# Kernel tuning notes

Measured on AMD Instinct MI355X. Metric: run time of the kernel, lower is better.

## Reference

```python
import jax, jax.numpy as jnp
import numpy as np

B, L, H, C, K, S = 32, 512, 336, 321, 8, 8   # batch, seq_len, pred_len, channels, leaders, states
FREQ = H // 2 + 1                            # 169
G = 2 * K + 1                                # filter groups
TEMP = 1.0
EPS = 1e-5


def setup_inputs() -> dict:
    key = jax.random.key(0)
    ks = jax.random.split(key, 12)
    x = jax.random.normal(ks[0], (B, L, C), jnp.float32)
    leader_ids = jax.random.randint(ks[1], (B, C, K), 0, C)
    shift = jax.random.randint(ks[2], (B, C, K), 0, L)
    r = jax.random.normal(ks[3], (B, C, K), jnp.float32)
    # backbone linear: seq_len -> pred_len
    Wb = jax.random.normal(ks[4], (H, L), jnp.float32) * float(1.0 / np.sqrt(L))
    bb = jnp.zeros((H,), jnp.float32)
    # factory classifier: (L + K) features -> state_num logits
    Wc = jax.random.normal(ks[5], (S, L + K), jnp.float32) * float(1.0 / np.sqrt(L + K))
    bc = jnp.zeros((S,), jnp.float32)
    # state prototype filters (complex, stored as re/im): [S, 2K+1, FREQ]
    states_re = jax.random.normal(ks[6], (S, G, FREQ), jnp.float32) * float(1.0 / np.sqrt(S))
    states_im = jax.random.normal(ks[7], (S, G, FREQ), jnp.float32) * float(1.0 / np.sqrt(S))
    # complex mix layer: 3*FREQ -> FREQ
    Wm_re = jax.random.normal(ks[8], (FREQ, 3 * FREQ), jnp.float32) * float(1.0 / np.sqrt(3 * FREQ))
    Wm_im = jax.random.normal(ks[9], (FREQ, 3 * FREQ), jnp.float32) * float(1.0 / np.sqrt(3 * FREQ))
    bm_re = jnp.zeros((FREQ,), jnp.float32)
    bm_im = jnp.zeros((FREQ,), jnp.float32)
    return dict(x=x, r=r, Wb=Wb, bb=bb, Wc=Wc, bc=bc,
                states_re=states_re, states_im=states_im,
                Wm_re=Wm_re, Wm_im=Wm_im, bm_re=bm_re, bm_im=bm_im,
                leader_ids=leader_ids, shift=shift)


def reference(x, r, Wb, bb, Wc, bc, states_re, states_im, Wm_re, Wm_im, bm_re, bm_im, leader_ids, shift):
    xc = jnp.transpose(x, (0, 2, 1))                      # [B,C,L]
    mu = xc.mean(-1, keepdims=True)
    norm = jnp.sqrt(xc.var(-1, keepdims=True) + EPS)
    xn = (xc - mu) / norm                                 # instance_norm
    y_hat = jnp.einsum('bcl,hl->bch', xn, Wb) + bb        # backbone [B,C,H]

    # --- shifted_leader_seq (torch.no_grad) ---
    full = jax.lax.stop_gradient(jnp.concatenate([xn, y_hat], -1))      # [B,C,L+H]
    lead_full = full[jnp.arange(B)[:, None, None], leader_ids]          # [B,C,K,L+H]
    t_idx = (L - shift)[..., None] + jnp.arange(H)                      # [B,C,K,H]
    seq_shifted = jnp.take_along_axis(lead_full, t_idx, axis=-1)        # [B,C,K,H]
    r = jax.lax.stop_gradient(r)

    # softmax leader weights with leading constant-one slot
    ones = jnp.ones((B, C, 1), xn.dtype)
    r_soft = jax.nn.softmax(jnp.concatenate([ones, jnp.abs(r)], -1) / TEMP, axis=-1)  # [B,C,K+1]

    # --- factory: state-mixed complex filters ---
    feat = jnp.concatenate([xn, r_soft[..., 1:]], -1)                   # [B,C,L+K]
    p = jax.nn.softmax(jnp.einsum('bcf,sf->bcs', feat, Wc) + bc, axis=-1)
    states = states_re + 1j * states_im                                 # [S,G,FREQ]
    filters = jnp.einsum('bcs,sgf->bcgf', p, states)                    # [B,C,2K+1,FREQ]

    # --- FFT filter multiply-sum + inverse FFT mix ---
    y_hat_f = jnp.fft.rfft(y_hat)                                       # [B,C,FREQ]
    seq_shifted_f = jnp.fft.rfft(seq_shifted) * filters[:, :, :K]       # [B,C,K,FREQ]
    seq_diff_f = (seq_shifted_f - y_hat_f[:, :, None]) * filters[:, :, K:-1]
    yh_f = y_hat_f * filters[:, :, -1]
    z = jnp.concatenate([seq_shifted_f.sum(2), seq_diff_f.sum(2), yh_f], -1)  # [B,C,3*FREQ]
    Wm = Wm_re + 1j * Wm_im
    mixed = jnp.einsum('bcf,gf->bcg', z, Wm) + (bm_re + 1j * bm_im)     # [B,C,FREQ]
    y_hat = y_hat + jnp.fft.irfft(mixed, n=H)

    y = y_hat * norm + mu
    return jnp.transpose(y, (0, 2, 1))                                  # [B,H,C]
```

## Files before the change

kernel.cpp:

```cpp
#include <hip/hip_runtime.h>
#include <math.h>

#define B_ 32
#define L_ 512
#define H_ 336
#define C_ 321
#define K_ 8
#define S_ 8
#define FREQ_ 169
#define G_ 17
#define LHB_ 848
#define F_FEAT 520
#define EPS_ 1e-5f
#define BCN_ (B_ * C_)
#define DZB_ 7

#ifndef M_PIf
#define M_PIf 3.14159265358979323846f
#endif

typedef __attribute__((ext_vector_type(8))) short short8v;
typedef __attribute__((ext_vector_type(4))) float f32x4;

__device__ __forceinline__ unsigned short f2bf(float x) {
    unsigned u = __builtin_bit_cast(unsigned, x);
    u += 0x7FFFu + ((u >> 16) & 1u);
    return (unsigned short)(u >> 16);
}
__device__ __forceinline__ float bf2f(unsigned short h) {
    return __builtin_bit_cast(float, (unsigned)h << 16);
}


__global__ void k_prep_dft(unsigned short* __restrict__ T) {
    int blk = blockIdx.x, kc = blk / 22, nt = blk % 22, lane = threadIdx.x;
    int n = nt * 16 + (lane & 15);
    int kb = kc * 32 + (lane >> 4) * 8;
    int f = n >> 1;
    unsigned short* dst = T + (size_t)blk * 512 + lane * 8;
    for (int i = 0; i < 8; ++i) {
        int k = kb + i;
        float val = 0.f;
        if (k < H_ && n < 2 * FREQ_) {
            int m = (k * f) % H_;
            float s, c;
            sincosf((float)m * (2.0f * M_PIf / (float)H_), &s, &c);
            val = (n & 1) ? -s : c;
        }
        dst[i] = f2bf(val);
    }
}

__global__ __launch_bounds__(256) void k_prep_tab(float* __restrict__ ctb,
                                                  float* __restrict__ stb) {
    int idx = blockIdx.x * 256 + threadIdx.x;
    if (idx >= FREQ_ * H_) return;
    int g = idx / H_, h = idx % H_;
    int m = (g * h) % H_;
    float s, c;
    sincosf((float)m * (2.0f * M_PIf / (float)H_), &s, &c);
    float wgt = ((g == 0 || g == FREQ_ - 1) ? 1.0f : 2.0f) * (1.0f / (float)H_);
    ctb[idx] = wgt * c;
    stb[idx] = -wgt * s;
}

__global__ __launch_bounds__(256) void k_prep_wt3(const float* __restrict__ Wm_re,
                                                  const float* __restrict__ Wm_im,
                                                  const float* __restrict__ ctb,
                                                  const float* __restrict__ stb,
                                                  unsigned short* __restrict__ T) {
    int t = blockIdx.x * 256 + threadIdx.x;
    if (t >= 512 * H_) return;
    int k = t / H_, h = t - k * H_;
    float s1 = 0.f, s2 = 0.f;
    if (k < 3 * FREQ_) {
        #pragma unroll 4
        for (int g = 0; g < FREQ_; ++g) {
            float ct = ctb[g * H_ + h];
            float st = stb[g * H_ + h];
            float wr = Wm_re[(size_t)g * (3 * FREQ_) + k];
            float wi = Wm_im[(size_t)g * (3 * FREQ_) + k];
            s1 += wr * ct + wi * st;
            s2 += wr * st - wi * ct;
        }
    }
    int nt = h >> 4, nr = h & 15;
    {
        int kc = k >> 5, kr = k & 31;
        int lane = ((kr >> 3) << 4) | nr;
        T[((size_t)(kc * 21 + nt)) * 512 + lane * 8 + (k & 7)] = f2bf(s1);
    }
    {
        int kk = k + 512;
        int kc = kk >> 5, kr = kk & 31;
        int lane = ((kr >> 3) << 4) | nr;
        T[((size_t)(kc * 21 + nt)) * 512 + lane * 8 + (kk & 7)] = f2bf(s2);
    }
}

__global__ __launch_bounds__(64) void k_prep_bv(const float* __restrict__ bm_re,
                                                const float* __restrict__ bm_im,
                                                const float* __restrict__ ctb,
                                                const float* __restrict__ stb,
                                                float* __restrict__ bvec) {
    int h = blockIdx.x * 64 + threadIdx.x;
    if (h >= H_) return;
    float acc = 0.f;
    for (int g = 0; g < FREQ_; ++g)
        acc += bm_re[g] * ctb[g * H_ + h] + bm_im[g] * stb[g * H_ + h];
    bvec[h] = acc;
}

__global__ void k_prep_wb(const float* __restrict__ Wb, unsigned short* __restrict__ T) {
    int blk = blockIdx.x, kc = blk / 21, nt = blk % 21, lane = threadIdx.x;
    int n = nt * 16 + (lane & 15);
    int kb = kc * 32 + (lane >> 4) * 8;
    unsigned short* dst = T + (size_t)blk * 512 + lane * 8;
    for (int i = 0; i < 8; ++i) {
        int k = kb + i;
        dst[i] = f2bf(Wb[(size_t)n * L_ + k]);
    }
}

__global__ __launch_bounds__(256) void k_prep_st2(const float* __restrict__ st_re,
                                                  const float* __restrict__ st_im,
                                                  float4* __restrict__ stf4,
                                                  float2* __restrict__ stg3) {
    int idx = blockIdx.x * 256 + threadIdx.x;
    if (idx < 64 * FREQ_) {
        int row = idx / FREQ_, f = idx % FREQ_;
        int k = row >> 3, s = row & 7;
        size_t b1 = (size_t)s * (G_ * FREQ_) + (size_t)k * FREQ_ + f;
        size_t b2 = (size_t)s * (G_ * FREQ_) + (size_t)(8 + k) * FREQ_ + f;
        stf4[idx] = make_float4(st_re[b1], st_im[b1], st_re[b2], st_im[b2]);
    }
    if (idx < 8 * FREQ_) {
        int s = idx / FREQ_, f = idx % FREQ_;
        size_t b3 = (size_t)s * (G_ * FREQ_) + (size_t)16 * FREQ_ + f;
        stg3[idx] = make_float2(st_re[b3], st_im[b3]);
    }
}

__global__ __launch_bounds__(256) void k_stats_part(const float* __restrict__ x,
                                                    float2* __restrict__ part) {
    __shared__ float red_s[4][64], red_q[4][64];
    int tid = threadIdx.x, w = tid >> 6, lane = tid & 63;
    int b = blockIdx.y, c0 = blockIdx.x * 64, l0 = blockIdx.z * 64;
    int c = c0 + lane;
    bool valid = (c < C_);
    const float* xb = x + ((size_t)b * L_) * C_;
    float s = 0.f, q = 0.f;
    for (int li = w; li < 64; li += 4) {
        float v = valid ? xb[(size_t)(l0 + li) * C_ + c] : 0.f;
        s += v; q += v * v;
    }
    red_s[w][lane] = s; red_q[w][lane] = q;
    __syncthreads();
    if (w == 0) {
        float S = red_s[0][lane] + red_s[1][lane] + red_s[2][lane] + red_s[3][lane];
        float Q = red_q[0][lane] + red_q[1][lane] + red_q[2][lane] + red_q[3][lane];
        part[(size_t)(((b * 6 + blockIdx.x) * 8) + blockIdx.z) * 64 + lane] = make_float2(S, Q);
    }
}

__global__ __launch_bounds__(256) void k_stats_fin(const float2* __restrict__ part,
                                                   float* __restrict__ muv,
                                                   float* __restrict__ nrm) {
    int t = blockIdx.x * 256 + threadIdx.x;
    int b = t / 384, rem = t % 384;
    int ct = rem / 64, cl = rem % 64;
    int c = ct * 64 + cl;
    if (b >= B_ || c >= C_) return;
    float S = 0.f, Q = 0.f;
    #pragma unroll
    for (int ls = 0; ls < 8; ++ls) {
        float2 p = part[(size_t)(((b * 6 + ct) * 8) + ls) * 64 + cl];
        S += p.x; Q += p.y;
    }
    float mu = S / (float)L_;
    float var = Q / (float)L_ - mu * mu;
    float n = sqrtf(var + EPS_);
    muv[(size_t)b * C_ + c] = mu;
    nrm[(size_t)b * C_ + c] = n;
}

__global__ __launch_bounds__(256) void k_norm(const float* __restrict__ x,
                                              const float* __restrict__ muv,
                                              const float* __restrict__ nrm,
                                              unsigned short* __restrict__ fullbf) {
    __shared__ float tl[64][65];
    int tid = threadIdx.x, w = tid >> 6, lane = tid & 63;
    int b = blockIdx.y, c0 = blockIdx.x * 64, l0 = blockIdx.z * 64;
    int c = c0 + lane;
    bool valid = (c < C_);
    const float* xb = x + ((size_t)b * L_) * C_;
    float mu = valid ? muv[(size_t)b * C_ + c] : 0.f;
    float inv = valid ? (1.0f / nrm[(size_t)b * C_ + c]) : 0.f;
    for (int li = w; li < 64; li += 4) {
        float v = valid ? xb[(size_t)(l0 + li) * C_ + c] : 0.f;
        tl[li][lane] = (v - mu) * inv;
    }
    __syncthreads();
    for (int cr = w; cr < 64; cr += 4) {
        int cc = c0 + cr;
        if (cc < C_ && lane < 32) {
            size_t bc = (size_t)b * C_ + cc;
            unsigned pk = (unsigned)f2bf(tl[2 * lane][cr]) |
                          ((unsigned)f2bf(tl[2 * lane + 1][cr]) << 16);
            ((unsigned*)fullbf)[(bc * LHB_ + l0) / 2 + lane] = pk;
        }
    }
}

__global__ __launch_bounds__(256) void k_yhat(const unsigned short* __restrict__ fullbf_r,
                                              const unsigned short* __restrict__ Wbsw,
                                              const float* __restrict__ bb,
                                              unsigned short* __restrict__ fullbf_w,
                                              float* __restrict__ yhf) {
    int bc0 = blockIdx.x * 32;
    int half = blockIdx.y;
    int tid = threadIdx.x, w = tid >> 6, lane = tid & 63;
    const int NTB0[5] = {0, 3, 6, 9, 11};
    const int NTB1[5] = {11, 14, 17, 19, 21};
    int nt0 = half ? NTB1[w] : NTB0[w];
    int ntn = (half ? NTB1[w + 1] : NTB0[w + 1]) - nt0;
    int r15 = lane & 15, kg = lane >> 4;
    f32x4 acc[2][3];
    #pragma unroll
    for (int mf = 0; mf < 2; ++mf)
        #pragma unroll
        for (int j = 0; j < 3; ++j) acc[mf][j] = (f32x4){0.f, 0.f, 0.f, 0.f};
    for (int kc = 0; kc < 16; ++kc) {
        short8v a[2];
        #pragma unroll
        for (int mf = 0; mf < 2; ++mf)
            a[mf] = *(const short8v*)(fullbf_r + ((size_t)(bc0 + mf * 16 + r15) * LHB_ + kc * 32 + kg * 8));
        #pragma unroll
        for (int j = 0; j < 3; ++j) {
            if (j >= ntn) continue;
            short8v bfr = *(const short8v*)(Wbsw + ((size_t)(kc * 21 + nt0 + j) * 512 + lane * 8));
            #pragma unroll
            for (int mf = 0; mf < 2; ++mf)
                acc[mf][j] = __builtin_amdgcn_mfma_f32_16x16x32_bf16(a[mf], bfr, acc[mf][j], 0, 0, 0);
        }
    }
    #pragma unroll
    for (int mf = 0; mf < 2; ++mf)
        #pragma unroll
        for (int j = 0; j < 3; ++j) {
            if (j >= ntn) continue;
            int n_ = (nt0 + j) * 16 + r15;
            #pragma unroll
            for (int reg = 0; reg < 4; ++reg) {
                int bc = bc0 + mf * 16 + kg * 4 + reg;
                float v = acc[mf][j][reg] + bb[n_];
                fullbf_w[(size_t)bc * LHB_ + L_ + n_] = f2bf(v);
                yhf[(size_t)bc * H_ + n_] = v;
            }
        }
}

__global__ __launch_bounds__(256) void k_p2(const unsigned short* __restrict__ fullbf,
                                            const float* __restrict__ r,
                                            const float* __restrict__ Wc,
                                            const float* __restrict__ bcv,
                                            float* __restrict__ p_out) {
    __shared__ float WcS[8 * F_FEAT];
    __shared__ float rsS[16][8];
    __shared__ float bcS[8];
    int tid = threadIdx.x, w = tid >> 6, lane = tid & 63;
    int bc0 = blockIdx.x * 16;
    for (int i = tid; i < 8 * F_FEAT; i += 256) WcS[i] = Wc[i];
    if (tid < 8) bcS[tid] = bcv[tid];
    if (tid < 16) {
        int bc = bc0 + tid;
        const float* rr = r + (size_t)bc * K_;
        float a[8]; float m = 1.0f;
        #pragma unroll
        for (int k = 0; k < 8; ++k) { a[k] = fabsf(rr[k]); m = fmaxf(m, a[k]); }
        float Z = expf(1.0f - m);
        float e[8];
        #pragma unroll
        for (int k = 0; k < 8; ++k) { e[k] = expf(a[k] - m); Z += e[k]; }
        float inv = 1.0f / Z;
        #pragma unroll
        for (int k = 0; k < 8; ++k) rsS[tid][k] = e[k] * inv;
    }
    __syncthreads();

    for (int i = 0; i < 4; ++i) {
        int bcl = w * 4 + i;
        int bc = bc0 + bcl;
        const unsigned* xrow = (const unsigned*)(fullbf + (size_t)bc * LHB_);
        float acc[8] = {0.f, 0.f, 0.f, 0.f, 0.f, 0.f, 0.f, 0.f};
        #pragma unroll
        for (int t = 0; t < 4; ++t) {
            int j = lane + t * 64;
            unsigned v = xrow[j];
            float x0 = bf2f((unsigned short)(v & 0xffff));
            float x1 = bf2f((unsigned short)(v >> 16));
            #pragma unroll
            for (int s = 0; s < 8; ++s)
                acc[s] += x0 * WcS[s * F_FEAT + 2 * j] + x1 * WcS[s * F_FEAT + 2 * j + 1];
        }
        if (lane < 8) {
            float xf = rsS[bcl][lane];
            #pragma unroll
            for (int s = 0; s < 8; ++s) acc[s] += xf * WcS[s * F_FEAT + L_ + lane];
        }
        #pragma unroll
        for (int s = 0; s < 8; ++s) {
            #pragma unroll
            for (int off = 32; off > 0; off >>= 1) acc[s] += __shfl_down(acc[s], off);
        }
        if (lane == 0) {
            float m = -1e30f;
            #pragma unroll
            for (int s = 0; s < 8; ++s) { acc[s] += bcS[s]; m = fmaxf(m, acc[s]); }
            float Z = 0.f; float e[8];
            #pragma unroll
            for (int s = 0; s < 8; ++s) { e[s] = expf(acc[s] - m); Z += e[s]; }
            float inv = 1.0f / Z;
            #pragma unroll
            for (int s = 0; s < 8; ++s) p_out[(size_t)bc * 8 + s] = e[s] * inv;
        }
    }
}

__global__ __launch_bounds__(512) void k_dftz2(const unsigned short* __restrict__ fullbf,
                                               const int* __restrict__ leader,
                                               const int* __restrict__ shiftp,
                                               const unsigned short* __restrict__ Tsw,
                                               const float* __restrict__ pbuf,
                                               const float4* __restrict__ stf4,
                                               const float2* __restrict__ stg3,
                                               unsigned short* __restrict__ zbf) {
    __shared__ unsigned short A[64 * 360];
    __shared__ float psL[DZB_][8];
    int tid = threadIdx.x, w = tid >> 6, lane = tid & 63;
    int bc0 = blockIdx.x * DZB_;
    unsigned* A32 = (unsigned*)A;
    for (int i = tid; i < 64 * 180; i += 512) A32[i] = 0;
    if (tid < DZB_ * 8) {
        int bcl = tid >> 3, s = tid & 7;
        int bc = bc0 + bcl;
        psL[bcl][s] = (bc < BCN_) ? pbuf[(size_t)bc * 8 + s] : 0.f;
    }
    __syncthreads();

    #pragma unroll
    for (int i = 0; i < 8; ++i) {
        int rr = w * 8 + i;
        if (rr >= 63) break;
        int bcl = rr / 9, k = rr - bcl * 9;
        int bc = bc0 + bcl;
        if (bc < BCN_) {
            int b = bc / C_;
            const unsigned short* src;
            if (k < 8) {
                int lead = leader[(size_t)bc * K_ + k];
                int sh = shiftp[(size_t)bc * K_ + k];
                src = fullbf + ((size_t)b * C_ + lead) * LHB_ + (L_ - sh);
            } else {
                src = fullbf + (size_t)bc * LHB_ + L_;
            }
            unsigned short* dst = A + rr * 360;
            #pragma unroll
            for (int t = 0; t < 6; ++t) {
                int j = lane + t * 64;
                if (j < H_) dst[j] = src[j];
            }
        }
    }
    __syncthreads();

    const int NTB[9] = {0, 3, 6, 9, 11, 14, 17, 20, 22};
    int nt0 = NTB[w], ntn = NTB[w + 1] - nt0;
    int r15 = lane & 15, kg = lane >> 4;
    f32x4 acc[4][3];
    #pragma unroll
    for (int mf = 0; mf < 4; ++mf)
        #pragma unroll
        for (int j = 0; j < 3; ++j) acc[mf][j] = (f32x4){0.f, 0.f, 0.f, 0.f};
    for (int kc = 0; kc < 11; ++kc) {
        short8v a[4];
        #pragma unroll
        for (int mf = 0; mf < 4; ++mf)
            a[mf] = *(const short8v*)(A + (size_t)(mf * 16 + r15) * 360 + kc * 32 + kg * 8);
        #pragma unroll
        for (int j = 0; j < 3; ++j) {
            if (j >= ntn) continue;
            short8v bfr = *(const short8v*)(Tsw + ((size_t)(kc * 22 + nt0 + j) * 512 + lane * 8));
            #pragma unroll
            for (int mf = 0; mf < 4; ++mf)
                acc[mf][j] = __builtin_amdgcn_mfma_f32_16x16x32_bf16(a[mf], bfr, acc[mf][j], 0, 0, 0);
        }
    }
    __syncthreads();

    #pragma unroll
    for (int mf = 0; mf < 4; ++mf)
        #pragma unroll
        for (int j = 0; j < 3; ++j) {
            if (j >= ntn) continue;
            int col = (nt0 + j) * 16 + r15;
            #pragma unroll
            for (int reg = 0; reg < 4; ++reg) {
                int row = mf * 16 + kg * 4 + reg;
                A[row * 360 + col] = f2bf(acc[mf][j][reg]);
            }
        }
    __syncthreads();

    if (tid < 338) {
        int g = (tid >= 169) ? 1 : 0;
        int f = tid - g * 169;
        int bclo = g * 4;
        int nb = g ? 3 : 4;
        float z1r[4], z1i[4], z2r[4], z2i[4], Yr[4], Yi[4];
        #pragma unroll
        for (int bl = 0; bl < 4; ++bl) {
            z1r[bl] = z1i[bl] = z2r[bl] = z2i[bl] = 0.f;
            int row = (bclo + bl) * 9 + 8;
            unsigned v = (bl < nb) ? A32[row * 180 + f] : 0u;
            Yr[bl] = bf2f((unsigned short)(v & 0xffff));
            Yi[bl] = bf2f((unsigned short)(v >> 16));
        }
        for (int k = 0; k < 8; ++k) {
            float4 stv[8];
            #pragma unroll
            for (int s = 0; s < 8; ++s) stv[s] = stf4[(size_t)(k * 8 + s) * FREQ_ + f];
            #pragma unroll
            for (int bl = 0; bl < 4; ++bl) {
                if (bl >= nb) continue;
                int bcl = bclo + bl;
                float f1r = 0.f, f1i = 0.f, f2r = 0.f, f2i = 0.f;
                #pragma unroll
                for (int s = 0; s < 8; ++s) {
                    float p = psL[bcl][s];
                    f1r += p * stv[s].x; f1i += p * stv[s].y;
                    f2r += p * stv[s].z; f2i += p * stv[s].w;
                }
                unsigned v = A32[(bcl * 9 + k) * 180 + f];
                float Xr = bf2f((unsigned short)(v & 0xffff));
                float Xi = bf2f((unsigned short)(v >> 16));
                float ar = Xr * f1r - Xi * f1i;
                float ai = Xr * f1i + Xi * f1r;
                z1r[bl] += ar; z1i[bl] += ai;
                float dr = ar - Yr[bl], di = ai - Yi[bl];
                z2r[bl] += dr * f2r - di * f2i;
                z2i[bl] += dr * f2i + di * f2r;
            }
        }
        #pragma unroll
        for (int bl = 0; bl < 4; ++bl) {
            if (bl >= nb) continue;
            int bcl = bclo + bl;
            int bc = bc0 + bcl;
            if (bc >= BCN_) continue;
            float f3r = 0.f, f3i = 0.f;
            #pragma unroll
            for (int s = 0; s < 8; ++s) {
                float2 v3 = stg3[(size_t)s * FREQ_ + f];
                float p = psL[bcl][s];
                f3r += p * v3.x; f3i += p * v3.y;
            }
            unsigned short* zrow = zbf + (size_t)bc * 1024;
            zrow[f]       = f2bf(z1r[bl]);  zrow[512 + f]       = f2bf(z1i[bl]);
            zrow[169 + f] = f2bf(z2r[bl]);  zrow[512 + 169 + f] = f2bf(z2i[bl]);
            zrow[338 + f] = f2bf(Yr[bl] * f3r - Yi[bl] * f3i);
            zrow[512 + 338 + f] = f2bf(Yr[bl] * f3i + Yi[bl] * f3r);
        }
    } else if (tid >= 344 && tid < 344 + DZB_ * 10) {
        int t = tid - 344;
        int bcl = t / 10, o = t - bcl * 10;
        int bc = bc0 + bcl;
        if (bc < BCN_) {
            unsigned short* zrow = zbf + (size_t)bc * 1024;
            if (o < 5) zrow[507 + o] = 0;
            else       zrow[1019 + (o - 5)] = 0;
        }
    }
}

__global__ __launch_bounds__(256) void k_mixf2(const unsigned short* __restrict__ zbf,
                                               const unsigned short* __restrict__ WTsw,
                                               const float* __restrict__ bvec,
                                               const float* __restrict__ yhf,
                                               const float* __restrict__ muv,
                                               const float* __restrict__ nrm,
                                               float* __restrict__ out) {
    __shared__ float ytile[32][177];
    int bc0 = blockIdx.x * 32;
    int half = blockIdx.y;
    int tid = threadIdx.x, w = tid >> 6, lane = tid & 63;
    const int NTB0[5] = {0, 3, 6, 9, 11};
    const int NTB1[5] = {11, 14, 17, 19, 21};
    int nt0 = half ? NTB1[w] : NTB0[w];
    int ntn = (half ? NTB1[w + 1] : NTB0[w + 1]) - nt0;
    int h0 = half ? 176 : 0;
    int hn = half ? 160 : 176;
    int r15 = lane & 15, kg = lane >> 4;
    f32x4 acc[2][3];
    #pragma unroll
    for (int mf = 0; mf < 2; ++mf)
        #pragma unroll
        for (int j = 0; j < 3; ++j) acc[mf][j] = (f32x4){0.f, 0.f, 0.f, 0.f};
    for (int kc = 0; kc < 32; ++kc) {
        short8v a[2];
        #pragma unroll
        for (int mf = 0; mf < 2; ++mf)
            a[mf] = *(const short8v*)(zbf + ((size_t)(bc0 + mf * 16 + r15) * 1024 + kc * 32 + kg * 8));
        #pragma unroll
        for (int j = 0; j < 3; ++j) {
            if (j >= ntn) continue;
            short8v bfr = *(const short8v*)(WTsw + ((size_t)(kc * 21 + nt0 + j) * 512 + lane * 8));
            #pragma unroll
            for (int mf = 0; mf < 2; ++mf)
                acc[mf][j] = __builtin_amdgcn_mfma_f32_16x16x32_bf16(a[mf], bfr, acc[mf][j], 0, 0, 0);
        }
    }
    #pragma unroll
    for (int mf = 0; mf < 2; ++mf)
        #pragma unroll
        for (int j = 0; j < 3; ++j) {
            if (j >= ntn) continue;
            int h = (nt0 + j) * 16 + r15;
            float bv = bvec[h];
            #pragma unroll
            for (int reg = 0; reg < 4; ++reg) {
                int bcl = mf * 16 + kg * 4 + reg;
                int bc = bc0 + bcl;
                float y = (yhf[(size_t)bc * H_ + h] + acc[mf][j][reg] + bv) * nrm[bc] + muv[bc];
                ytile[bcl][h - h0] = y;
            }
        }
    __syncthreads();
    for (int idx = tid; idx < 32 * hn; idx += 256) {
        int bcl = idx & 31, hrel = idx >> 5;
        int bc = bc0 + bcl;
        int b = bc / C_, c = bc - b * C_;
        out[((size_t)b * H_ + h0 + hrel) * C_ + c] = ytile[bcl][hrel];
    }
}

extern "C" void kernel_launch(void* const* d_in, const int* in_sizes, int n_in,
                              void* d_out, int out_size, void* d_ws, size_t ws_size,
                              hipStream_t stream) {
    const float* x     = (const float*)d_in[0];
    const float* r     = (const float*)d_in[1];
    const float* Wb    = (const float*)d_in[2];
    const float* bb    = (const float*)d_in[3];
    const float* Wc    = (const float*)d_in[4];
    const float* bcv   = (const float*)d_in[5];
    const float* st_re = (const float*)d_in[6];
    const float* st_im = (const float*)d_in[7];
    const float* Wm_re = (const float*)d_in[8];
    const float* Wm_im = (const float*)d_in[9];
    const float* bm_re = (const float*)d_in[10];
    const float* bm_im = (const float*)d_in[11];
    const int* leader  = (const int*)d_in[12];
    const int* shiftp  = (const int*)d_in[13];
    float* out = (float*)d_out;

    char* w = (char*)d_ws;
    auto carve = [&](size_t bytes) {
        char* p = w;
        w += (bytes + 255) & ~(size_t)255;
        return (void*)p;
    };
    unsigned short* Tdft = (unsigned short*)carve((size_t)11 * 22 * 512 * 2);
    unsigned short* WTsw = (unsigned short*)carve((size_t)32 * 21 * 512 * 2);
    unsigned short* Wbsw = (unsigned short*)carve((size_t)16 * 21 * 512 * 2);
    float*          ctb  = (float*)carve((size_t)FREQ_ * H_ * 4);
    float*          stb  = (float*)carve((size_t)FREQ_ * H_ * 4);
    float*          bvec = (float*)carve((size_t)H_ * 4);
    float4*         stf4 = (float4*)carve((size_t)64 * FREQ_ * 16);
    float2*         stg3 = (float2*)carve((size_t)8 * FREQ_ * 8);
    float2*         part = (float2*)carve((size_t)B_ * 6 * 8 * 64 * 8);
    unsigned short* fullbf = (unsigned short*)carve((size_t)BCN_ * LHB_ * 2);
    float*          yhf  = (float*)carve((size_t)BCN_ * H_ * 4);
    float*          muv  = (float*)carve((size_t)BCN_ * 4);
    float*          nrm  = (float*)carve((size_t)BCN_ * 4);
    float*          pbuf = (float*)carve((size_t)BCN_ * 8 * 4);
    unsigned short* zbf  = (unsigned short*)carve((size_t)BCN_ * 1024 * 2);

    hipLaunchKernelGGL(k_prep_dft, dim3(11 * 22), dim3(64), 0, stream, Tdft);
    hipLaunchKernelGGL(k_prep_tab, dim3((FREQ_ * H_ + 255) / 256), dim3(256), 0, stream, ctb, stb);
    hipLaunchKernelGGL(k_prep_wt3, dim3((512 * H_ + 255) / 256), dim3(256), 0, stream,
                       Wm_re, Wm_im, ctb, stb, WTsw);
    hipLaunchKernelGGL(k_prep_bv,  dim3((H_ + 63) / 64), dim3(64), 0, stream, bm_re, bm_im, ctb, stb, bvec);
    hipLaunchKernelGGL(k_prep_wb,  dim3(16 * 21), dim3(64), 0, stream, Wb, Wbsw);
    hipLaunchKernelGGL(k_prep_st2, dim3((64 * FREQ_ + 255) / 256), dim3(256), 0, stream,
                       st_re, st_im, stf4, stg3);
    hipLaunchKernelGGL(k_stats_part, dim3(6, 32, 8), dim3(256), 0, stream, x, part);
    hipLaunchKernelGGL(k_stats_fin, dim3(48), dim3(256), 0, stream, part, muv, nrm);
    hipLaunchKernelGGL(k_norm, dim3(6, 32, 8), dim3(256), 0, stream, x, muv, nrm, fullbf);
    hipLaunchKernelGGL(k_yhat, dim3(BCN_ / 32, 2), dim3(256), 0, stream, fullbf, Wbsw, bb, fullbf, yhf);
    hipLaunchKernelGGL(k_p2, dim3(BCN_ / 16), dim3(256), 0, stream, fullbf, r, Wc, bcv, pbuf);
    hipLaunchKernelGGL(k_dftz2, dim3((BCN_ + DZB_ - 1) / DZB_), dim3(512), 0, stream,
                       fullbf, leader, shiftp, Tdft, pbuf, stf4, stg3, zbf);
    hipLaunchKernelGGL(k_mixf2, dim3(BCN_ / 32, 2), dim3(256), 0, stream,
                       zbf, WTsw, bvec, yhf, muv, nrm, out);
}
```

Before: 242.4 us.

## Merge prep kernels, drop fp32 y_hat buffer, rebalance dftz2 thread mapping

```diff
diff --git a/kernel.cpp b/kernel.cpp
--- a/kernel.cpp
+++ b/kernel.cpp
@@ -31,113 +31,122 @@
     return __builtin_bit_cast(float, (unsigned)h << 16);
 }
 
-
-__global__ void k_prep_dft(unsigned short* __restrict__ T) {
-    int blk = blockIdx.x, kc = blk / 22, nt = blk % 22, lane = threadIdx.x;
-    int n = nt * 16 + (lane & 15);
-    int kb = kc * 32 + (lane >> 4) * 8;
-    int f = n >> 1;
-    unsigned short* dst = T + (size_t)blk * 512 + lane * 8;
-    for (int i = 0; i < 8; ++i) {
-        int k = kb + i;
-        float val = 0.f;
-        if (k < H_ && n < 2 * FREQ_) {
-            int m = (k * f) % H_;
+__global__ __launch_bounds__(256) void k_prepA(const float* __restrict__ Wb,
+                                               const float* __restrict__ st_re,
+                                               const float* __restrict__ st_im,
+                                               unsigned short* __restrict__ Tdft,
+                                               float* __restrict__ ctb,
+                                               float* __restrict__ stb,
+                                               unsigned short* __restrict__ Wbsw,
+                                               float4* __restrict__ stf4,
+                                               float2* __restrict__ stg3) {
+    int bid = blockIdx.x, tid = threadIdx.x;
+    if (bid < 61) {
+        int orig = bid * 4 + (tid >> 6);
+        if (orig < 11 * 22) {
+            int lane = tid & 63;
+            int kc = orig / 22, nt = orig % 22;
+            int n = nt * 16 + (lane & 15);
+            int kb = kc * 32 + (lane >> 4) * 8;
+            int f = n >> 1;
+            unsigned short* dst = Tdft + (size_t)orig * 512 + lane * 8;
+            for (int i = 0; i < 8; ++i) {
+                int k = kb + i;
+                float val = 0.f;
+                if (k < H_ && n < 2 * FREQ_) {
+                    int m = (k * f) % H_;
+                    float s, c;
+                    sincosf((float)m * (2.0f * M_PIf / (float)H_), &s, &c);
+                    val = (n & 1) ? -s : c;
+                }
+                dst[i] = f2bf(val);
+            }
+        }
+    } else if (bid < 283) {
+        int idx = (bid - 61) * 256 + tid;
+        if (idx < FREQ_ * H_) {
+            int g = idx / H_, h = idx % H_;
+            int m = (g * h) % H_;
             float s, c;
             sincosf((float)m * (2.0f * M_PIf / (float)H_), &s, &c);
-            val = (n & 1) ? -s : c;
-        }
-        dst[i] = f2bf(val);
-    }
-}
-
-__global__ __launch_bounds__(256) void k_prep_tab(float* __restrict__ ctb,
-                                                  float* __restrict__ stb) {
-    int idx = blockIdx.x * 256 + threadIdx.x;
-    if (idx >= FREQ_ * H_) return;
-    int g = idx / H_, h = idx % H_;
-    int m = (g * h) % H_;
-    float s, c;
-    sincosf((float)m * (2.0f * M_PIf / (float)H_), &s, &c);
-    float wgt = ((g == 0 || g == FREQ_ - 1) ? 1.0f : 2.0f) * (1.0f / (float)H_);
-    ctb[idx] = wgt * c;
-    stb[idx] = -wgt * s;
-}
-
-__global__ __launch_bounds__(256) void k_prep_wt3(const float* __restrict__ Wm_re,
-                                                  const float* __restrict__ Wm_im,
-                                                  const float* __restrict__ ctb,
-                                                  const float* __restrict__ stb,
-                                                  unsigned short* __restrict__ T) {
-    int t = blockIdx.x * 256 + threadIdx.x;
-    if (t >= 512 * H_) return;
-    int k = t / H_, h = t - k * H_;
-    float s1 = 0.f, s2 = 0.f;
-    if (k < 3 * FREQ_) {
-        #pragma unroll 4
-        for (int g = 0; g < FREQ_; ++g) {
-            float ct = ctb[g * H_ + h];
-            float st = stb[g * H_ + h];
-            float wr = Wm_re[(size_t)g * (3 * FREQ_) + k];
-            float wi = Wm_im[(size_t)g * (3 * FREQ_) + k];
-            s1 += wr * ct + wi * st;
-            s2 += wr * st - wi * ct;
-        }
-    }
-    int nt = h >> 4, nr = h & 15;
-    {
-        int kc = k >> 5, kr = k & 31;
-        int lane = ((kr >> 3) << 4) | nr;
-        T[((size_t)(kc * 21 + nt)) * 512 + lane * 8 + (k & 7)] = f2bf(s1);
-    }
-    {
-        int kk = k + 512;
-        int kc = kk >> 5, kr = kk & 31;
-        int lane = ((kr >> 3) << 4) | nr;
-        T[((size_t)(kc * 21 + nt)) * 512 + lane * 8 + (kk & 7)] = f2bf(s2);
-    }
-}
-
-__global__ __launch_bounds__(64) void k_prep_bv(const float* __restrict__ bm_re,
-                                                const float* __restrict__ bm_im,
-                                                const float* __restrict__ ctb,
-                                                const float* __restrict__ stb,
-                                                float* __restrict__ bvec) {
-    int h = blockIdx.x * 64 + threadIdx.x;
-    if (h >= H_) return;
-    float acc = 0.f;
-    for (int g = 0; g < FREQ_; ++g)
-        acc += bm_re[g] * ctb[g * H_ + h] + bm_im[g] * stb[g * H_ + h];
-    bvec[h] = acc;
-}
-
-__global__ void k_prep_wb(const float* __restrict__ Wb, unsigned short* __restrict__ T) {
-    int blk = blockIdx.x, kc = blk / 21, nt = blk % 21, lane = threadIdx.x;
-    int n = nt * 16 + (lane & 15);
-    int kb = kc * 32 + (lane >> 4) * 8;
-    unsigned short* dst = T + (size_t)blk * 512 + lane * 8;
-    for (int i = 0; i < 8; ++i) {
-        int k = kb + i;
-        dst[i] = f2bf(Wb[(size_t)n * L_ + k]);
-    }
-}
-
-__global__ __launch_bounds__(256) void k_prep_st2(const float* __restrict__ st_re,
-                                                  const float* __restrict__ st_im,
-                                                  float4* __restrict__ stf4,
-                                                  float2* __restrict__ stg3) {
-    int idx = blockIdx.x * 256 + threadIdx.x;
-    if (idx < 64 * FREQ_) {
-        int row = idx / FREQ_, f = idx % FREQ_;
-        int k = row >> 3, s = row & 7;
-        size_t b1 = (size_t)s * (G_ * FREQ_) + (size_t)k * FREQ_ + f;
-        size_t b2 = (size_t)s * (G_ * FREQ_) + (size_t)(8 + k) * FREQ_ + f;
-        stf4[idx] = make_float4(st_re[b1], st_im[b1], st_re[b2], st_im[b2]);
-    }
-    if (idx < 8 * FREQ_) {
-        int s = idx / FREQ_, f = idx % FREQ_;
-        size_t b3 = (size_t)s * (G_ * FREQ_) + (size_t)16 * FREQ_ + f;
-        stg3[idx] = make_float2(st_re[b3], st_im[b3]);
+            float wgt = ((g == 0 || g == FREQ_ - 1) ? 1.0f : 2.0f) * (1.0f / (float)H_);
+            ctb[idx] = wgt * c;
+            stb[idx] = -wgt * s;
+        }
+    } else if (bid < 367) {
+        int orig = (bid - 283) * 4 + (tid >> 6);
+        if (orig < 16 * 21) {
+            int lane = tid & 63;
+            int kc = orig / 21, nt = orig % 21;
+            int n = nt * 16 + (lane & 15);
+            int kb = kc * 32 + (lane >> 4) * 8;
+            unsigned short* dst = Wbsw + (size_t)orig * 512 + lane * 8;
+            for (int i = 0; i < 8; ++i) {
+                int k = kb + i;
+                dst[i] = f2bf(Wb[(size_t)n * L_ + k]);
+            }
+        }
+    } else {
+        int idx = (bid - 367) * 256 + tid;
+        if (idx < 64 * FREQ_) {
+            int row = idx / FREQ_, f = idx % FREQ_;
+            int k = row >> 3, s = row & 7;
+            size_t b1 = (size_t)s * (G_ * FREQ_) + (size_t)k * FREQ_ + f;
+            size_t b2 = (size_t)s * (G_ * FREQ_) + (size_t)(8 + k) * FREQ_ + f;
+            stf4[idx] = make_float4(st_re[b1], st_im[b1], st_re[b2], st_im[b2]);
+        }
+        if (idx < 8 * FREQ_) {
+            int s = idx / FREQ_, f = idx % FREQ_;
+            size_t b3 = (size_t)s * (G_ * FREQ_) + (size_t)16 * FREQ_ + f;
+            stg3[idx] = make_float2(st_re[b3], st_im[b3]);
+        }
+    }
+}
+
+__global__ __launch_bounds__(256) void k_prepB(const float* __restrict__ Wm_re,
+                                               const float* __restrict__ Wm_im,
+                                               const float* __restrict__ bm_re,
+                                               const float* __restrict__ bm_im,
+                                               const float* __restrict__ ctb,
+                                               const float* __restrict__ stb,
+                                               unsigned short* __restrict__ T,
+                                               float* __restrict__ bvec) {
+    int bid = blockIdx.x, tid = threadIdx.x;
+    if (bid < 672) {
+        int t = bid * 256 + tid;
+        if (t >= 512 * H_) return;
+        int k = t / H_, h = t - k * H_;
+        float s1 = 0.f, s2 = 0.f;
+        if (k < 3 * FREQ_) {
+            #pragma unroll 4
+            for (int g = 0; g < FREQ_; ++g) {
+                float ct = ctb[g * H_ + h];
+                float st = stb[g * H_ + h];
+                float wr = Wm_re[(size_t)g * (3 * FREQ_) + k];
+                float wi = Wm_im[(size_t)g * (3 * FREQ_) + k];
+                s1 += wr * ct + wi * st;
+                s2 += wr * st - wi * ct;
+            }
+        }
+        int nt = h >> 4, nr = h & 15;
+        {
+            int kc = k >> 5, kr = k & 31;
+            int lane = ((kr >> 3) << 4) | nr;
+            T[((size_t)(kc * 21 + nt)) * 512 + lane * 8 + (k & 7)] = f2bf(s1);
+        }
+        {
+            int kk = k + 512;
+            int kc = kk >> 5, kr = kk & 31;
+            int lane = ((kr >> 3) << 4) | nr;
+            T[((size_t)(kc * 21 + nt)) * 512 + lane * 8 + (kk & 7)] = f2bf(s2);
+        }
+    } else {
+        int h = (bid - 672) * 256 + tid;
+        if (h >= H_) return;
+        float acc = 0.f;
+        for (int g = 0; g < FREQ_; ++g)
+            acc += bm_re[g] * ctb[g * H_ + h] + bm_im[g] * stb[g * H_ + h];
+        bvec[h] = acc;
     }
 }
 
@@ -215,8 +224,7 @@
 __global__ __launch_bounds__(256) void k_yhat(const unsigned short* __restrict__ fullbf_r,
                                               const unsigned short* __restrict__ Wbsw,
                                               const float* __restrict__ bb,
-                                              unsigned short* __restrict__ fullbf_w,
-                                              float* __restrict__ yhf) {
+                                              unsigned short* __restrict__ fullbf_w) {
     int bc0 = blockIdx.x * 32;
     int half = blockIdx.y;
     int tid = threadIdx.x, w = tid >> 6, lane = tid & 63;
@@ -253,9 +261,7 @@
             #pragma unroll
             for (int reg = 0; reg < 4; ++reg) {
                 int bc = bc0 + mf * 16 + kg * 4 + reg;
-                float v = acc[mf][j][reg] + bb[n_];
-                fullbf_w[(size_t)bc * LHB_ + L_ + n_] = f2bf(v);
-                yhf[(size_t)bc * H_ + n_] = v;
+                fullbf_w[(size_t)bc * LHB_ + L_ + n_] = f2bf(acc[mf][j][reg] + bb[n_]);
             }
         }
 }
@@ -346,6 +352,16 @@
         int bc = bc0 + bcl;
         psL[bcl][s] = (bc < BCN_) ? pbuf[(size_t)bc * 8 + s] : 0.f;
     }
+    if (tid >= 64 && tid < 64 + DZB_ * 10) {
+        int t = tid - 64;
+        int bcl = t / 10, o = t - bcl * 10;
+        int bc = bc0 + bcl;
+        if (bc < BCN_) {
+            unsigned short* zrow = zbf + (size_t)bc * 1024;
+            if (o < 5) zrow[507 + o] = 0;
+            else       zrow[1019 + (o - 5)] = 0;
+        }
+    }
     __syncthreads();
 
     #pragma unroll
@@ -412,17 +428,16 @@
         }
     __syncthreads();
 
-    if (tid < 338) {
-        int g = (tid >= 169) ? 1 : 0;
+    if (tid < 507) {
+        int g = tid / 169;
         int f = tid - g * 169;
-        int bclo = g * 4;
-        int nb = g ? 3 : 4;
-        float z1r[4], z1i[4], z2r[4], z2i[4], Yr[4], Yi[4];
-        #pragma unroll
-        for (int bl = 0; bl < 4; ++bl) {
+        int bclo = (g == 0) ? 0 : (g == 1) ? 3 : 5;
+        int nb   = (g == 0) ? 3 : 2;
+        float z1r[3], z1i[3], z2r[3], z2i[3], Yr[3], Yi[3];
+        #pragma unroll
+        for (int bl = 0; bl < 3; ++bl) {
             z1r[bl] = z1i[bl] = z2r[bl] = z2i[bl] = 0.f;
-            int row = (bclo + bl) * 9 + 8;
-            unsigned v = (bl < nb) ? A32[row * 180 + f] : 0u;
+            unsigned v = (bl < nb) ? A32[((bclo + bl) * 9 + 8) * 180 + f] : 0u;
             Yr[bl] = bf2f((unsigned short)(v & 0xffff));
             Yi[bl] = bf2f((unsigned short)(v >> 16));
         }
@@ -431,7 +446,7 @@
             #pragma unroll
             for (int s = 0; s < 8; ++s) stv[s] = stf4[(size_t)(k * 8 + s) * FREQ_ + f];
             #pragma unroll
-            for (int bl = 0; bl < 4; ++bl) {
+            for (int bl = 0; bl < 3; ++bl) {
                 if (bl >= nb) continue;
                 int bcl = bclo + bl;
                 float f1r = 0.f, f1i = 0.f, f2r = 0.f, f2i = 0.f;
@@ -453,7 +468,7 @@
             }
         }
         #pragma unroll
-        for (int bl = 0; bl < 4; ++bl) {
+        for (int bl = 0; bl < 3; ++bl) {
             if (bl >= nb) continue;
             int bcl = bclo + bl;
             int bc = bc0 + bcl;
@@ -471,22 +486,13 @@
             zrow[338 + f] = f2bf(Yr[bl] * f3r - Yi[bl] * f3i);
             zrow[512 + 338 + f] = f2bf(Yr[bl] * f3i + Yi[bl] * f3r);
         }
-    } else if (tid >= 344 && tid < 344 + DZB_ * 10) {
-        int t = tid - 344;
-        int bcl = t / 10, o = t - bcl * 10;
-        int bc = bc0 + bcl;
-        if (bc < BCN_) {
-            unsigned short* zrow = zbf + (size_t)bc * 1024;
-            if (o < 5) zrow[507 + o] = 0;
-            else       zrow[1019 + (o - 5)] = 0;
-        }
     }
 }
 
 __global__ __launch_bounds__(256) void k_mixf2(const unsigned short* __restrict__ zbf,
                                                const unsigned short* __restrict__ WTsw,
                                                const float* __restrict__ bvec,
-                                               const float* __restrict__ yhf,
+                                               const unsigned short* __restrict__ fullbf,
                                                const float* __restrict__ muv,
                                                const float* __restrict__ nrm,
                                                float* __restrict__ out) {
@@ -531,7 +537,8 @@
             for (int reg = 0; reg < 4; ++reg) {
                 int bcl = mf * 16 + kg * 4 + reg;
                 int bc = bc0 + bcl;
-                float y = (yhf[(size_t)bc * H_ + h] + acc[mf][j][reg] + bv) * nrm[bc] + muv[bc];
+                float yh = bf2f(fullbf[(size_t)bc * LHB_ + L_ + h]);
+                float y = (yh + acc[mf][j][reg] + bv) * nrm[bc] + muv[bc];
                 ytile[bcl][h - h0] = y;
             }
         }
@@ -579,27 +586,22 @@
     float2*         stg3 = (float2*)carve((size_t)8 * FREQ_ * 8);
     float2*         part = (float2*)carve((size_t)B_ * 6 * 8 * 64 * 8);
     unsigned short* fullbf = (unsigned short*)carve((size_t)BCN_ * LHB_ * 2);
-    float*          yhf  = (float*)carve((size_t)BCN_ * H_ * 4);
     float*          muv  = (float*)carve((size_t)BCN_ * 4);
     float*          nrm  = (float*)carve((size_t)BCN_ * 4);
     float*          pbuf = (float*)carve((size_t)BCN_ * 8 * 4);
     unsigned short* zbf  = (unsigned short*)carve((size_t)BCN_ * 1024 * 2);
 
-    hipLaunchKernelGGL(k_prep_dft, dim3(11 * 22), dim3(64), 0, stream, Tdft);
-    hipLaunchKernelGGL(k_prep_tab, dim3((FREQ_ * H_ + 255) / 256), dim3(256), 0, stream, ctb, stb);
-    hipLaunchKernelGGL(k_prep_wt3, dim3((512 * H_ + 255) / 256), dim3(256), 0, stream,
-                       Wm_re, Wm_im, ctb, stb, WTsw);
-    hipLaunchKernelGGL(k_prep_bv,  dim3((H_ + 63) / 64), dim3(64), 0, stream, bm_re, bm_im, ctb, stb, bvec);
-    hipLaunchKernelGGL(k_prep_wb,  dim3(16 * 21), dim3(64), 0, stream, Wb, Wbsw);
-    hipLaunchKernelGGL(k_prep_st2, dim3((64 * FREQ_ + 255) / 256), dim3(256), 0, stream,
-                       st_re, st_im, stf4, stg3);
+    hipLaunchKernelGGL(k_prepA, dim3(410), dim3(256), 0, stream,
+                       Wb, st_re, st_im, Tdft, ctb, stb, Wbsw, stf4, stg3);
+    hipLaunchKernelGGL(k_prepB, dim3(674), dim3(256), 0, stream,
+                       Wm_re, Wm_im, bm_re, bm_im, ctb, stb, WTsw, bvec);
     hipLaunchKernelGGL(k_stats_part, dim3(6, 32, 8), dim3(256), 0, stream, x, part);
     hipLaunchKernelGGL(k_stats_fin, dim3(48), dim3(256), 0, stream, part, muv, nrm);
     hipLaunchKernelGGL(k_norm, dim3(6, 32, 8), dim3(256), 0, stream, x, muv, nrm, fullbf);
-    hipLaunchKernelGGL(k_yhat, dim3(BCN_ / 32, 2), dim3(256), 0, stream, fullbf, Wbsw, bb, fullbf, yhf);
+    hipLaunchKernelGGL(k_yhat, dim3(BCN_ / 32, 2), dim3(256), 0, stream, fullbf, Wbsw, bb, fullbf);
     hipLaunchKernelGGL(k_p2, dim3(BCN_ / 16), dim3(256), 0, stream, fullbf, r, Wc, bcv, pbuf);
     hipLaunchKernelGGL(k_dftz2, dim3((BCN_ + DZB_ - 1) / DZB_), dim3(512), 0, stream,
                        fullbf, leader, shiftp, Tdft, pbuf, stf4, stg3, zbf);
     hipLaunchKernelGGL(k_mixf2, dim3(BCN_ / 32, 2), dim3(256), 0, stream,
-                       zbf, WTsw, bvec, yhf, muv, nrm, out);
-}
+                       zbf, WTsw, bvec, fullbf, muv, nrm, out);
+}
```

New measurement: 226.2 us. 1.07x faster.
